# Optimization experiments

Measured on AMD Instinct MI355X. Metric: run time of the kernel, lower is better.

## Reference

```python
import jax, jax.numpy as jnp
import numpy as np
from jax.scipy.special import i0

B, P = 2, 524288
N = (512, 512)            # uniform frequency grid
M = 4                     # window cutoff m (2M taps per dim)
SIGMA = 2.0
NGRID = tuple(2 * (int(SIGMA * Ni) // 2) for Ni in N)  # oversampled grid (1024, 1024)
BETA = tuple(float(np.pi * (2.0 - 1.0 / (ng / Ni))) for ng, Ni in zip(NGRID, N))


def _phi_hat_1d(Ni, ni, b):
    # Fourier coefficients of the Kaiser-Bessel window, k = -Ni/2 .. Ni/2-1
    k = jnp.arange(-Ni // 2, Ni // 2, dtype=jnp.float32)
    arg = jnp.sqrt(b * b - (2.0 * jnp.pi * k / ni) ** 2)
    return i0(M * arg) / ni


def _window_ft():
    # separable d-dim Fourier coefficient grid, shape [N1, N2] (== window.ft)
    c1 = _phi_hat_1d(N[0], NGRID[0], BETA[0])
    c2 = _phi_hat_1d(N[1], NGRID[1], BETA[1])
    return c1[:, None] * c2[None, :]


def _phi(t, ni, b):
    # Kaiser-Bessel window in time domain, support |t| <= M/ni
    u2 = M * M - (ni * t) ** 2
    u = jnp.sqrt(jnp.maximum(u2, 1e-12))
    return jnp.where(u2 > 0, jnp.sinh(b * u) / (jnp.pi * u), 0.0)


def setup_inputs() -> dict:
    key = jax.random.key(0)
    k1, k2 = jax.random.split(key)
    x = jax.random.uniform(k1, (B, P, 2), jnp.float32, -0.5, 0.5)  # points on torus
    f_hat = jax.random.normal(k2, (B, N[0], N[1], 2), jnp.float32)  # complex as [re,im]
    return {"x": x, "f_hat": f_hat}


def _nfft_forward(x, f_hat):
    # f(x_j) ~= sum_k f_hat[k] exp(-2 pi i <k, x_j>) via window-deconvolved oversampled FFT + local gather
    fh = (f_hat[..., 0] + 1j * f_hat[..., 1]).astype(jnp.complex64)  # [B, N1, N2]
    ft = _window_ft().astype(jnp.float32)
    gh = fh / ft                                                    # deconvolve
    p1 = (NGRID[0] - N[0]) // 2
    p2 = (NGRID[1] - N[1]) // 2
    gh = jnp.pad(gh, ((0, 0), (p1, p1), (p2, p2)))                  # centered zero-pad to n
    g = jnp.fft.fftn(jnp.fft.ifftshift(gh, axes=(-2, -1)), axes=(-2, -1))
    g = g / (NGRID[0] * NGRID[1])                                   # g_l = (1/n) sum_k gh_k e^{-2pi i kl/n}

    offs = jnp.arange(-M + 1, M + 1)                                # [2M]
    ws, idxs = [], []
    for d in range(2):
        nd = NGRID[d]
        xd = x[..., d]                                              # [B, P]
        l0 = jnp.floor(xd * nd).astype(jnp.int32)
        l = l0[..., None] + offs                                    # [B, P, 2M]
        t = xd[..., None] - l.astype(jnp.float32) / nd
        ws.append(_phi(t, nd, BETA[d]))
        idxs.append(jnp.mod(l, nd))

    g_flat = g.reshape(B, NGRID[0] * NGRID[1])
    acc = jnp.zeros((B, P), jnp.complex64)
    for i in range(2 * M):                                          # fixed 2m x 2m taps
        for j in range(2 * M):
            flat = idxs[0][..., i] * NGRID[1] + idxs[1][..., j]     # [B, P]
            gv = jnp.take_along_axis(g_flat, flat, axis=1)
            acc = acc + (ws[0][..., i] * ws[1][..., j]) * gv
    return jnp.stack([acc.real, acc.imag], axis=-1)                 # [B, P, 2]


def reference(x, f_hat):
    return _nfft_forward(x, f_hat)
```

## Files before the change

### kernel.cpp

```cpp
#include <hip/hip_runtime.h>

constexpr int   BATCH = 2;
constexpr int   NPTS  = 524288;
constexpr int   BINS  = 2048;
constexpr int   CAP   = 768;
constexpr float BETA  = 4.71238898038469f;
constexpr float PI_F  = 3.14159265358979f;

typedef float v2f __attribute__((ext_vector_type(2)));

#define PIDX(i) ((i) + ((i) >> 4))

constexpr size_t G_BYTES  = (size_t)BATCH * 1024 * 1024 * sizeof(v2f);
constexpr size_t GCNT_OFF = G_BYTES;
constexpr size_t PERM_OFF = G_BYTES + 8192;

__device__ __forceinline__ float i0f_large(float x) {
    float t = 3.75f / x;
    float p =  0.00392377f;
    p = p * t + -0.01647633f;
    p = p * t +  0.02635537f;
    p = p * t + -0.02057706f;
    p = p * t +  0.00916281f;
    p = p * t + -0.00157565f;
    p = p * t +  0.00225319f;
    p = p * t +  0.01328592f;
    p = p * t +  0.39894228f;
    return __expf(x) * rsqrtf(x) * p;
}

__device__ __forceinline__ int tile_of(v2f xv, int b) {
    int c1 = ((int)floorf(xv.x * 1024.0f)) & 1023;
    int c2 = ((int)floorf(xv.y * 1024.0f)) & 1023;
    return (b << 10) + ((c1 >> 5) << 5) + (c2 >> 5);
}

__device__ __forceinline__ v2f cmul4(v2f a, float4 t) {
    v2f lo = {t.x, t.y}, hi = {t.z, t.w};
    return a.x * lo + a.y * hi;
}
__device__ __forceinline__ v2f irot(v2f b) { return (v2f){-b.y, b.x}; }
__device__ __forceinline__ v2f cmulv(v2f a, v2f b) {
    return (v2f){a.x * b.x - a.y * b.y, a.x * b.y + a.y * b.x};
}
__device__ __forceinline__ float4 tw4p(v2f w) {
    return make_float4(w.x, w.y, -w.y, w.x);
}

__device__ __forceinline__ int digitrev4_10(int f) {
    unsigned r = __brev((unsigned)f) >> 22;
    return (int)(((r & 0x2AAu) >> 1) | ((r & 0x155u) << 1));
}

__device__ __forceinline__ void build_tw_small(float4* T, int tid, int nthreads,
                                               int q0, int sig0, int nst) {
    int off = 0, q = q0, sig = sig0;
    for (int st = 0; st < nst; ++st) {
        for (int m = tid; m < 3 * q; m += nthreads) {
            int sec = m / q, j = m - sec * q;
            float ang = (-2.0f * PI_F / 1024.0f) * (float)((sec + 1) * j * sig);
            float sw, cw;
            __sincosf(ang, &sw, &cw);
            T[off + m] = make_float4(cw, sw, -sw, cw);
        }
        off += 3 * q; q >>= 2; sig <<= 2;
    }
}

__device__ __forceinline__ void bfly4(v2f* s, const float4* T,
                                      int bt, int q, int off) {
    int j    = bt & (q - 1);
    int base = ((bt - j) << 2) + j;
    int p0 = PIDX(base), p1 = PIDX(base + q);
    int p2 = PIDX(base + 2 * q), p3 = PIDX(base + 3 * q);
    v2f a0 = s[p0], a1 = s[p1], a2 = s[p2], a3 = s[p3];
    v2f t0 = a0 + a2, t1 = a0 - a2, t2 = a1 + a3, t3 = a1 - a3;
    v2f r3 = irot(t3);
    s[p0] = t0 + t2;
    s[p1] = cmul4(t1 - r3, T[off + j]);
    s[p2] = cmul4(t0 - t2, T[off + q + j]);
    s[p3] = cmul4(t1 + r3, T[off + 2 * q + j]);
}

__global__ __launch_bounds__(256) void rows_and_bin(const v2f* __restrict__ fh,
                                                    v2f* __restrict__ g,
                                                    const v2f* __restrict__ x,
                                                    int* __restrict__ gcnt,
                                                    float4* __restrict__ perm) {
    __shared__ __align__(16) char smem[12784];
    int tid = threadIdx.x;

    if (blockIdx.x < 1024) {
        if (blockIdx.x == 0) {
            #pragma unroll
            for (int i = 0; i < 8; ++i)
                atomicExch(&gcnt[tid * 8 + i], 0);
        }
        v2f*    s = (v2f*)smem;
        float4* T = (float4*)(smem + 8704);
        int blk = blockIdx.x & 511;
        int b   = blockIdx.x >> 9;
        int row = (blk < 256) ? blk : blk + 512;
        int a1  = (row + 256) & 1023;

        build_tw_small(T, tid, 256, 64, 4, 4);

        float k1 = (float)(a1 - 256);
        float w1 = (2.0f * PI_F / 1024.0f) * k1;
        float c1 = i0f_large(4.0f * sqrtf(BETA * BETA - w1 * w1));

        const v2f* fr = fh + ((long)b << 18) + ((long)a1 << 9);

        float w2a = (2.0f * PI_F / 1024.0f) * (float)tid;
        float c2a = i0f_large(4.0f * sqrtf(BETA * BETA - w2a * w2a));
        float w2b = (2.0f * PI_F / 1024.0f) * (float)(tid - 256);
        float c2b = i0f_large(4.0f * sqrtf(BETA * BETA - w2b * w2b));

        v2f A = fr[tid + 256] * (1.0f / (c1 * c2a));
        v2f B = fr[tid]       * (1.0f / (c1 * c2b));

        float sw0, cw0;
        __sincosf((-2.0f * PI_F / 1024.0f) * (float)tid, &sw0, &cw0);
        v2f wt = {cw0, sw0};
        v2f wt2 = cmulv(wt, wt);
        v2f wt3 = cmulv(wt2, wt);

        __syncthreads();

        v2f rB = irot(B);
        s[PIDX(tid)]       = A + B;
        s[PIDX(tid + 256)] = cmul4(A + rB, tw4p(wt));
        s[PIDX(tid + 512)] = cmul4(A - B,  tw4p(wt2));
        s[PIDX(tid + 768)] = cmul4(A - rB, tw4p(wt3));

        int off = 0, q = 64;
        #pragma unroll
        for (int st = 0; st < 4; ++st) {
            __syncthreads();
            bfly4(s, T, tid, q, off);
            off += 3 * q; q >>= 2;
        }
        __syncthreads();

        v2f* base = g + ((long)b << 20) + ((long)row << 10);
        #pragma unroll
        for (int i = 0; i < 4; ++i) {
            int idx = tid + (i << 8);
            base[idx] = s[PIDX(digitrev4_10(idx))];
        }
    } else {
        int* h = (int*)smem;
        int bblk = blockIdx.x - 1024;
        for (int i = tid; i < BINS; i += 256) h[i] = 0;
        __syncthreads();

        int base = bblk * 2048;
        int tile[8];
        v2f pv[8];
        #pragma unroll
        for (int i = 0; i < 8; ++i) {
            int gid = base + tid + i * 256;
            pv[i]   = x[gid];
            tile[i] = tile_of(pv[i], gid >> 19);
            atomicAdd(&h[tile[i]], 1);
        }
        __syncthreads();

        #pragma unroll
        for (int j = 0; j < 8; ++j) {
            int bi = tid + j * 256;
            int c  = h[bi];
            h[bi]  = c ? atomicAdd(&gcnt[bi], c) : 0;
        }
        __syncthreads();

        #pragma unroll
        for (int i = 0; i < 8; ++i) {
            int gid = base + tid + i * 256;
            int pos = atomicAdd(&h[tile[i]], 1);
            perm[tile[i] * CAP + pos] =
                make_float4(pv[i].x, pv[i].y, __int_as_float(gid), 0.0f);
        }
    }
}

__global__ __launch_bounds__(256) void fft_cols(v2f* __restrict__ g) {
    constexpr int STR = 1092;
    __shared__ v2f    s[4 * STR];
    __shared__ float4 Tsm[60];
    int b  = blockIdx.y;
    int C0 = blockIdx.x * 4;
    int t  = threadIdx.x;
    int c  = t & 3, L = t >> 2;
    v2f* gb = g + ((long)b << 20);

    build_tw_small(Tsm, t, 256, 16, 16, 2);

    v2f E[16];
    #pragma unroll
    for (int m = 0; m < 4; ++m) {
        int r = L + 64 * m;
        E[m] = gb[((long)r << 10) + C0 + c];
    }
    #pragma unroll
    for (int m = 12; m < 16; ++m) {
        int r = L + 64 * m;
        E[m] = gb[((long)r << 10) + C0 + c];
    }

    float sL, cL;
    __sincosf((-2.0f * PI_F / 1024.0f) * (float)L, &sL, &cL);
    v2f wL = {cL, sL};
    const v2f R1 = {0.923879533f, -0.382683432f};
    const v2f R2 = {0.707106781f, -0.707106781f};
    const v2f R3 = {0.382683432f, -0.923879533f};

    #pragma unroll
    for (int m = 0; m < 4; ++m) {
        v2f w1 = (m == 0) ? wL : cmulv(wL, (m == 1) ? R1 : (m == 2) ? R2 : R3);
        v2f w2 = cmulv(w1, w1);
        v2f w3 = cmulv(w2, w1);
        v2f A = E[m], B = E[m + 12];
        v2f rB = irot(B);
        E[m]      = A + B;
        E[m + 4]  = cmul4(A + rB, tw4p(w1));
        E[m + 8]  = cmul4(A - B,  tw4p(w2));
        E[m + 12] = cmul4(A - rB, tw4p(w3));
    }

    {
        v2f p  = cmulv(wL, wL); p = cmulv(p, p);
        v2f p2 = cmulv(p, p);
        v2f p3 = cmulv(p2, p);
        float4 u1 = tw4p(p), u2 = tw4p(p2), u3 = tw4p(p3);
        #pragma unroll
        for (int a = 0; a < 4; ++a) {
            v2f a0 = E[4*a], a1 = E[4*a+1], a2 = E[4*a+2], a3 = E[4*a+3];
            v2f t0 = a0 + a2, t1 = a0 - a2, t2 = a1 + a3, t3 = a1 - a3;
            v2f r3 = irot(t3);
            E[4*a]   = t0 + t2;
            E[4*a+1] = cmul4(t1 - r3, u1);
            E[4*a+2] = cmul4(t0 - t2, u2);
            E[4*a+3] = cmul4(t1 + r3, u3);
        }
    }

    __syncthreads();
    v2f* sf = s + c * STR;
    #pragma unroll
    for (int m = 0; m < 16; ++m) sf[PIDX(L + 64 * m)] = E[m];
    __syncthreads();

    #pragma unroll
    for (int rr = 0; rr < 4; ++rr)
        bfly4(sf, Tsm, L + rr * 64, 16, 0);
    __syncthreads();

    v2f C[16];
    int cb = 17 * L;
    #pragma unroll
    for (int j = 0; j < 16; ++j) C[j] = sf[cb + j];

    #pragma unroll
    for (int j = 0; j < 4; ++j) {
        v2f a0 = C[j], a1 = C[j+4], a2 = C[j+8], a3 = C[j+12];
        v2f t0 = a0 + a2, t1 = a0 - a2, t2 = a1 + a3, t3 = a1 - a3;
        v2f r3 = irot(t3);
        C[j]    = t0 + t2;
        C[j+4]  = cmul4(t1 - r3, Tsm[48 + j]);
        C[j+8]  = cmul4(t0 - t2, Tsm[52 + j]);
        C[j+12] = cmul4(t1 + r3, Tsm[56 + j]);
    }
    #pragma unroll
    for (int e = 0; e < 4; ++e) {
        v2f a0 = C[4*e], a1 = C[4*e+1], a2 = C[4*e+2], a3 = C[4*e+3];
        v2f t0 = a0 + a2, t1 = a0 - a2, t2 = a1 + a3, t3 = a1 - a3;
        v2f r3 = irot(t3);
        C[4*e]   = t0 + t2;
        C[4*e+1] = t1 - r3;
        C[4*e+2] = t0 - t2;
        C[4*e+3] = t1 + r3;
    }

    #pragma unroll
    for (int j = 0; j < 16; ++j) {
        int r = digitrev4_10((L << 4) + j);
        gb[((long)r << 10) + C0 + c] = C[j];
    }
}

__global__ __launch_bounds__(256) void gather_binned(const v2f* __restrict__ g,
                                                     const int* __restrict__ gcnt,
                                                     const float4* __restrict__ perm,
                                                     v2f* __restrict__ out) {
    __shared__ v2f patch[37 * 37];
    int tb = blockIdx.x;
    int b  = tb >> 10;
    int tt = tb & 1023;
    int tR = tt >> 5, tC = tt & 31;
    int R0 = (tR << 5) - 2, C0 = (tC << 5) - 2;
    const v2f* gb = g + ((long)b << 20);

    for (int p = threadIdx.x; p < 37 * 37; p += 256) {
        int pr = p / 37, pc = p - pr * 37;
        int gr = (R0 + pr) & 1023, gc = (C0 + pc) & 1023;
        patch[p] = gb[(gr << 10) + gc];
    }
    __syncthreads();

    int cnt = gcnt[tb];
    if (cnt > CAP) cnt = CAP;
    int off0 = tb * CAP;
    for (int i = (int)threadIdx.x; i < cnt; i += 256) {
        float4 rec = perm[off0 + i];
        int gid = __float_as_int(rec.z);

        float w1[6], w2[6];
        int rr0, cc0;
        {
            float xs = rec.x * 1024.0f;
            float fl = floorf(xs);
            float fr = xs - fl;
            rr0 = (((int)fl) & 1023) - (tR << 5);
            #pragma unroll
            for (int k = 0; k < 6; ++k) {
                float tv = fr - (float)(k - 2);
                float u2 = 16.0f - tv * tv;
                float ir = rsqrtf(u2);
                float z  = BETA * u2 * ir;
                w1[k] = __expf(z) * 0.159154943f * ir;
            }
        }
        {
            float xs = rec.y * 1024.0f;
            float fl = floorf(xs);
            float fr = xs - fl;
            cc0 = (((int)fl) & 1023) - (tC << 5);
            #pragma unroll
            for (int k = 0; k < 6; ++k) {
                float tv = fr - (float)(k - 2);
                float u2 = 16.0f - tv * tv;
                float ir = rsqrtf(u2);
                float z  = BETA * u2 * ir;
                w2[k] = __expf(z) * 0.159154943f * ir;
            }
        }

        v2f acc = {0.0f, 0.0f};
        #pragma unroll
        for (int ii = 0; ii < 6; ++ii) {
            int pbase = (rr0 + ii) * 37 + cc0;
            float wi = w1[ii];
            #pragma unroll
            for (int jj = 0; jj < 6; ++jj)
                acc += (wi * w2[jj]) * patch[pbase + jj];
        }
        out[gid] = acc;
    }
}

extern "C" void kernel_launch(void* const* d_in, const int* in_sizes, int n_in,
                              void* d_out, int out_size, void* d_ws, size_t ws_size,
                              hipStream_t stream) {
    const v2f* x  = (const v2f*)d_in[0];
    const v2f* fh = (const v2f*)d_in[1];
    char* ws = (char*)d_ws;
    v2f*    g    = (v2f*)ws;
    int*    gcnt = (int*)(ws + GCNT_OFF);
    float4* perm = (float4*)(ws + PERM_OFF);

    rows_and_bin<<<dim3(1536), dim3(256), 0, stream>>>(fh, g, x, gcnt, perm);
    fft_cols    <<<dim3(256, BATCH), dim3(256), 0, stream>>>(g);

    gather_binned<<<dim3(BINS), dim3(256), 0, stream>>>(g, gcnt, perm, (v2f*)d_out);
}
```

Before: 117.2 us.

## Process both batches per row-FFT block, double binning work, split perm records

```diff
diff --git a/kernel.cpp b/kernel.cpp
--- a/kernel.cpp
+++ b/kernel.cpp
@@ -13,7 +13,8 @@
 
 constexpr size_t G_BYTES  = (size_t)BATCH * 1024 * 1024 * sizeof(v2f);
 constexpr size_t GCNT_OFF = G_BYTES;
-constexpr size_t PERM_OFF = G_BYTES + 8192;
+constexpr size_t PXY_OFF  = G_BYTES + 8192;
+constexpr size_t PID_OFF  = PXY_OFF + (size_t)BINS * CAP * sizeof(v2f);
 
 __device__ __forceinline__ float i0f_large(float x) {
     float t = 3.75f / x;
@@ -86,11 +87,12 @@
                                                     v2f* __restrict__ g,
                                                     const v2f* __restrict__ x,
                                                     int* __restrict__ gcnt,
-                                                    float4* __restrict__ perm) {
+                                                    v2f* __restrict__ pxy,
+                                                    int* __restrict__ pid) {
     __shared__ __align__(16) char smem[12784];
     int tid = threadIdx.x;
 
-    if (blockIdx.x < 1024) {
+    if (blockIdx.x < 512) {
         if (blockIdx.x == 0) {
             #pragma unroll
             for (int i = 0; i < 8; ++i)
@@ -98,8 +100,7 @@
         }
         v2f*    s = (v2f*)smem;
         float4* T = (float4*)(smem + 8704);
-        int blk = blockIdx.x & 511;
-        int b   = blockIdx.x >> 9;
+        int blk = blockIdx.x;
         int row = (blk < 256) ? blk : blk + 512;
         int a1  = (row + 256) & 1023;
 
@@ -108,57 +109,64 @@
         float k1 = (float)(a1 - 256);
         float w1 = (2.0f * PI_F / 1024.0f) * k1;
         float c1 = i0f_large(4.0f * sqrtf(BETA * BETA - w1 * w1));
-
-        const v2f* fr = fh + ((long)b << 18) + ((long)a1 << 9);
 
         float w2a = (2.0f * PI_F / 1024.0f) * (float)tid;
         float c2a = i0f_large(4.0f * sqrtf(BETA * BETA - w2a * w2a));
         float w2b = (2.0f * PI_F / 1024.0f) * (float)(tid - 256);
         float c2b = i0f_large(4.0f * sqrtf(BETA * BETA - w2b * w2b));
-
-        v2f A = fr[tid + 256] * (1.0f / (c1 * c2a));
-        v2f B = fr[tid]       * (1.0f / (c1 * c2b));
+        float ia = 1.0f / (c1 * c2a);
+        float ib = 1.0f / (c1 * c2b);
+
+        const v2f* fr0 = fh + ((long)a1 << 9);
+        const v2f* fr1 = fr0 + (1L << 18);
+        v2f A0 = fr0[tid + 256], B0 = fr0[tid];
+        v2f A1 = fr1[tid + 256], B1 = fr1[tid];
+        A0 *= ia; B0 *= ib; A1 *= ia; B1 *= ib;
 
         float sw0, cw0;
         __sincosf((-2.0f * PI_F / 1024.0f) * (float)tid, &sw0, &cw0);
         v2f wt = {cw0, sw0};
-        v2f wt2 = cmulv(wt, wt);
-        v2f wt3 = cmulv(wt2, wt);
-
-        __syncthreads();
-
-        v2f rB = irot(B);
-        s[PIDX(tid)]       = A + B;
-        s[PIDX(tid + 256)] = cmul4(A + rB, tw4p(wt));
-        s[PIDX(tid + 512)] = cmul4(A - B,  tw4p(wt2));
-        s[PIDX(tid + 768)] = cmul4(A - rB, tw4p(wt3));
-
-        int off = 0, q = 64;
-        #pragma unroll
-        for (int st = 0; st < 4; ++st) {
+        float4 t1p = tw4p(wt);
+        float4 t2p = tw4p(cmulv(wt, wt));
+        float4 t3p = tw4p(cmulv(cmulv(wt, wt), wt));
+
+        #pragma unroll
+        for (int b = 0; b < 2; ++b) {
+            v2f A = b ? A1 : A0, B = b ? B1 : B0;
             __syncthreads();
-            bfly4(s, T, tid, q, off);
-            off += 3 * q; q >>= 2;
-        }
-        __syncthreads();
-
-        v2f* base = g + ((long)b << 20) + ((long)row << 10);
-        #pragma unroll
-        for (int i = 0; i < 4; ++i) {
-            int idx = tid + (i << 8);
-            base[idx] = s[PIDX(digitrev4_10(idx))];
+            v2f rB = irot(B);
+            s[PIDX(tid)]       = A + B;
+            s[PIDX(tid + 256)] = cmul4(A + rB, t1p);
+            s[PIDX(tid + 512)] = cmul4(A - B,  t2p);
+            s[PIDX(tid + 768)] = cmul4(A - rB, t3p);
+
+            int off = 0, q = 64;
+            #pragma unroll
+            for (int st = 0; st < 4; ++st) {
+                __syncthreads();
+                bfly4(s, T, tid, q, off);
+                off += 3 * q; q >>= 2;
+            }
+            __syncthreads();
+
+            v2f* base = g + ((long)b << 20) + ((long)row << 10);
+            #pragma unroll
+            for (int i = 0; i < 4; ++i) {
+                int idx = tid + (i << 8);
+                base[idx] = s[PIDX(digitrev4_10(idx))];
+            }
         }
     } else {
         int* h = (int*)smem;
-        int bblk = blockIdx.x - 1024;
+        int bblk = blockIdx.x - 512;
         for (int i = tid; i < BINS; i += 256) h[i] = 0;
         __syncthreads();
 
-        int base = bblk * 2048;
-        int tile[8];
-        v2f pv[8];
-        #pragma unroll
-        for (int i = 0; i < 8; ++i) {
+        int base = bblk * 4096;
+        int tile[16];
+        v2f pv[16];
+        #pragma unroll
+        for (int i = 0; i < 16; ++i) {
             int gid = base + tid + i * 256;
             pv[i]   = x[gid];
             tile[i] = tile_of(pv[i], gid >> 19);
@@ -175,11 +183,12 @@
         __syncthreads();
 
         #pragma unroll
-        for (int i = 0; i < 8; ++i) {
-            int gid = base + tid + i * 256;
-            int pos = atomicAdd(&h[tile[i]], 1);
-            perm[tile[i] * CAP + pos] =
-                make_float4(pv[i].x, pv[i].y, __int_as_float(gid), 0.0f);
+        for (int i = 0; i < 16; ++i) {
+            int gid  = base + tid + i * 256;
+            int pos  = atomicAdd(&h[tile[i]], 1);
+            int slot = tile[i] * CAP + pos;
+            pxy[slot] = pv[i];
+            pid[slot] = gid;
         }
     }
 }
@@ -291,7 +300,8 @@
 
 __global__ __launch_bounds__(256) void gather_binned(const v2f* __restrict__ g,
                                                      const int* __restrict__ gcnt,
-                                                     const float4* __restrict__ perm,
+                                                     const v2f* __restrict__ pxy,
+                                                     const int* __restrict__ pid,
                                                      v2f* __restrict__ out) {
     __shared__ v2f patch[37 * 37];
     int tb = blockIdx.x;
@@ -312,13 +322,13 @@
     if (cnt > CAP) cnt = CAP;
     int off0 = tb * CAP;
     for (int i = (int)threadIdx.x; i < cnt; i += 256) {
-        float4 rec = perm[off0 + i];
-        int gid = __float_as_int(rec.z);
+        v2f xv  = pxy[off0 + i];
+        int gid = pid[off0 + i];
 
         float w1[6], w2[6];
         int rr0, cc0;
         {
-            float xs = rec.x * 1024.0f;
+            float xs = xv.x * 1024.0f;
             float fl = floorf(xs);
             float fr = xs - fl;
             rr0 = (((int)fl) & 1023) - (tR << 5);
@@ -332,7 +342,7 @@
             }
         }
         {
-            float xs = rec.y * 1024.0f;
+            float xs = xv.y * 1024.0f;
             float fl = floorf(xs);
             float fr = xs - fl;
             cc0 = (((int)fl) & 1023) - (tC << 5);
@@ -365,12 +375,14 @@
     const v2f* x  = (const v2f*)d_in[0];
     const v2f* fh = (const v2f*)d_in[1];
     char* ws = (char*)d_ws;
-    v2f*    g    = (v2f*)ws;
-    int*    gcnt = (int*)(ws + GCNT_OFF);
-    float4* perm = (float4*)(ws + PERM_OFF);
-
-    rows_and_bin<<<dim3(1536), dim3(256), 0, stream>>>(fh, g, x, gcnt, perm);
+    v2f* g    = (v2f*)ws;
+    int* gcnt = (int*)(ws + GCNT_OFF);
+    v2f* pxy  = (v2f*)(ws + PXY_OFF);
+    int* pid  = (int*)(ws + PID_OFF);
+
+    rows_and_bin<<<dim3(768), dim3(256), 0, stream>>>(fh, g, x, gcnt, pxy, pid);
     fft_cols    <<<dim3(256, BATCH), dim3(256), 0, stream>>>(g);
 
-    gather_binned<<<dim3(BINS), dim3(256), 0, stream>>>(g, gcnt, perm, (v2f*)d_out);
-}
+    gather_binned<<<dim3(BINS), dim3(256), 0, stream>>>(g, gcnt, pxy, pid,
+                                                        (v2f*)d_out);
+}
```

New measurement: 126.7 us. 1.08x slower.
